# Performance work log

Hardware: AMD Instinct MI355X
Metric: run time of the kernel (lower is better)

The kernel has to match this reference:

```python
import jax, jax.numpy as jnp
import numpy as np

B, S, D, H, R, P = 4, 8192, 512, 8, 64, 4
HD = D // H  # 64
EPS = 1e-6


def _sketch_p4(z, G1, G2):
    # sketchwithnegativity(z, 2): M1 = M2 = z
    inv_sqrt_r = 1.0 / np.sqrt(R).astype(np.float32)
    half = inv_sqrt_r * ((z @ G1) * (z @ G2))  # [B,H,S,R]
    return half * half  # sketch(): half * half for p=4


def setup_inputs() -> dict:
    key = jax.random.key(0)
    ks = jax.random.split(key, 16)
    lin = lambda k: jax.random.normal(k, (D, D), jnp.float32) * (1.0 / np.sqrt(D))
    g = lambda k: jax.random.normal(k, (HD, R), jnp.float32) * (1.0 / np.sqrt(R))
    return {
        "x": jax.random.normal(ks[0], (B, S, D), jnp.float32),
        "Wq": lin(ks[1]), "bq": jnp.zeros((D,), jnp.float32),
        "Wk": lin(ks[2]), "bk": jnp.zeros((D,), jnp.float32),
        "Wv": lin(ks[3]), "bv": jnp.zeros((D,), jnp.float32),
        "Wp": lin(ks[4]), "bp": jnp.zeros((D,), jnp.float32),
        "gamma_q": jnp.ones((1,), jnp.float32), "beta_q": jnp.zeros((1,), jnp.float32),
        "gamma_k": jnp.ones((1,), jnp.float32), "beta_k": jnp.zeros((1,), jnp.float32),
        "qG1": g(ks[5]), "qG2": g(ks[6]),
        "kG1": g(ks[7]), "kG2": g(ks[8]),
    }


def reference(x, Wq, bq, Wk, bk, Wv, bv, Wp, bp,
              gamma_q, beta_q, gamma_k, beta_k, qG1, qG2, kG1, kG2):
    b, s, d = x.shape
    split = lambda t: t.reshape(b, s, H, HD).transpose(0, 2, 1, 3)  # [B,H,S,HD]
    q = split(x @ Wq + bq)
    k = split(x @ Wk + bk)
    v = split(x @ Wv + bv)
    q = gamma_q * q + beta_q
    k = gamma_k * k + beta_k
    phi_q = _sketch_p4(q, qG1, qG2)  # [B,H,S,R]
    phi_k = _sketch_p4(k, kG1, kG2)  # [B,H,S,R]
    # linear-attention form of attn = (phi_q phi_k^T) / rowsum; avoids [S,S]
    kv = jnp.einsum('bhsr,bhsd->bhrd', phi_k, v)          # [B,H,R,HD]
    ksum = phi_k.sum(axis=2)                              # [B,H,R]
    num = jnp.einsum('bhqr,bhrd->bhqd', phi_q, kv)        # [B,H,S,HD]
    den = jnp.einsum('bhqr,bhr->bhq', phi_q, ksum) + EPS  # [B,H,S]
    out = num / den[..., None]
    out = out.transpose(0, 2, 1, 3).reshape(b, s, d)
    return out @ Wp + bp
```

## Files before the change

kernel.cpp:

```cpp
#include <hip/hip_runtime.h>
#include <hip/hip_bf16.h>


#define SEQ 8192

typedef __attribute__((ext_vector_type(8))) short bf16x8;
typedef __attribute__((ext_vector_type(4))) float f32x4;

__device__ __forceinline__ unsigned short f2b(float f) {
    union { float f; unsigned int i; } v; v.f = f;
    unsigned int r = v.i + 0x7fffu + ((v.i >> 16) & 1u);
    return (unsigned short)(r >> 16);
}

#if __has_builtin(__builtin_amdgcn_global_load_lds)
#define ASYNC_CP 1
#endif

__device__ __forceinline__ void cp16(const unsigned short* g, unsigned short* l) {
#ifdef ASYNC_CP
    __builtin_amdgcn_global_load_lds(
        (const __attribute__((address_space(1))) unsigned int*)g,
        (__attribute__((address_space(3))) unsigned int*)l, 16, 0, 0);
#endif
}

__global__ __launch_bounds__(256) void convert_x(
    const float* __restrict__ x, unsigned short* __restrict__ xb)
{
    size_t i = ((size_t)blockIdx.x * 256 + threadIdx.x) * 8;
    float4 a = *(const float4*)&x[i];
    float4 b = *(const float4*)&x[i + 4];
    ushort4 o1 = { f2b(a.x), f2b(a.y), f2b(a.z), f2b(a.w) };
    ushort4 o2 = { f2b(b.x), f2b(b.y), f2b(b.z), f2b(b.w) };
    *(ushort4*)&xb[i]     = o1;
    *(ushort4*)&xb[i + 4] = o2;
}

__global__ __launch_bounds__(256) void convert_wT(
    const float* __restrict__ Wq, const float* __restrict__ Wk,
    const float* __restrict__ Wv, const float* __restrict__ Wp,
    unsigned short* __restrict__ WT)
{
    const int z = blockIdx.z;
    const float* W = (z == 0) ? Wq : (z == 1) ? Wk : (z == 2) ? Wv : Wp;
    unsigned short* O = WT + (size_t)z * 262144;
    __shared__ float t[32][33];
    const int tid = threadIdx.x;
    const int tx = tid & 31, ty = tid >> 5;
    const int k0 = blockIdx.x * 32, n0 = blockIdx.y * 32;
    #pragma unroll
    for (int i = 0; i < 4; ++i)
        t[ty + 8 * i][tx] = W[(size_t)(k0 + ty + 8 * i) * 512 + n0 + tx];
    __syncthreads();
    #pragma unroll
    for (int i = 0; i < 4; ++i)
        O[(size_t)(n0 + ty + 8 * i) * 512 + k0 + tx] = f2b(t[tx][ty + 8 * i]);
}

__global__ __launch_bounds__(256) void gemm_mfma_qkv(
    const unsigned short* __restrict__ xb,
    const unsigned short* __restrict__ WT,
    const float* __restrict__ bq, const float* __restrict__ bk,
    const float* __restrict__ bvp,
    const float* __restrict__ gq, const float* __restrict__ bbq,
    const float* __restrict__ gk, const float* __restrict__ bbk,
    float* __restrict__ Q, float* __restrict__ Ko, float* __restrict__ Vo)
{
    const int z = blockIdx.z;
    const unsigned short* Wt = WT + (size_t)z * 262144;
    const float* bias = (z == 0) ? bq : (z == 1) ? bk : bvp;
    float g = 1.0f, be = 0.0f;
    if (z == 0)      { g = gq[0]; be = bbq[0]; }
    else if (z == 1) { g = gk[0]; be = bbk[0]; }
    float* C = (z == 0) ? Q : (z == 1) ? Ko : Vo;

    __shared__ __align__(16) unsigned short As[128 * 32];
    __shared__ __align__(16) unsigned short Bs[128 * 32];

    const int tid = threadIdx.x;
    const int w = tid >> 6, lane = tid & 63;
    const int n0 = blockIdx.x * 128;
    const int j0 = blockIdx.y * 128;
    const int wr = w >> 1, wc = w & 1;

    const int r0 = w * 32 + (lane >> 2);
    const int kq = (lane & 3) * 8;
    const unsigned short* gA = &xb[(size_t)(n0 + r0) * 512 + kq];
    const unsigned short* gB = &Wt[(size_t)(j0 + r0) * 512 + kq];
    unsigned short* lA = &As[(w * 32) * 32];
    unsigned short* lB = &Bs[(w * 32) * 32];

    f32x4 acc[4][4];
    #pragma unroll
    for (int i = 0; i < 4; ++i)
        #pragma unroll
        for (int j = 0; j < 4; ++j) { acc[i][j] = (f32x4){0.f, 0.f, 0.f, 0.f}; }

    for (int k0 = 0; k0 < 512; k0 += 32) {
        __syncthreads();
#ifdef ASYNC_CP
        cp16(gA + k0, lA);
        cp16(gA + 16 * 512 + k0, lA + 16 * 32);
        cp16(gB + k0, lB);
        cp16(gB + 16 * 512 + k0, lB + 16 * 32);
#else
        { uint4 v = *(const uint4*)(gA + k0);            *(uint4*)(lA + (size_t)lane * 8) = v; }
        { uint4 v = *(const uint4*)(gA + 16 * 512 + k0); *(uint4*)(lA + 16 * 32 + (size_t)lane * 8) = v; }
        { uint4 v = *(const uint4*)(gB + k0);            *(uint4*)(lB + (size_t)lane * 8) = v; }
        { uint4 v = *(const uint4*)(gB + 16 * 512 + k0); *(uint4*)(lB + 16 * 32 + (size_t)lane * 8) = v; }
#endif
        __syncthreads();

        bf16x8 af[4], bfr[4];
        #pragma unroll
        for (int i = 0; i < 4; ++i) {
            af[i]  = *(const bf16x8*)&As[(wr * 64 + i * 16 + (lane & 15)) * 32 + (lane >> 4) * 8];
            bfr[i] = *(const bf16x8*)&Bs[(wc * 64 + i * 16 + (lane & 15)) * 32 + (lane >> 4) * 8];
        }
        #pragma unroll
        for (int mi = 0; mi < 4; ++mi)
            #pragma unroll
            for (int ni = 0; ni < 4; ++ni)
                acc[mi][ni] = __builtin_amdgcn_mfma_f32_16x16x32_bf16(
                    af[mi], bfr[ni], acc[mi][ni], 0, 0, 0);
    }

    #pragma unroll
    for (int ni = 0; ni < 4; ++ni) {
        const int jcol = j0 + wc * 64 + ni * 16 + (lane & 15);
        const float bv = bias[jcol];
        const int h = jcol >> 6, hd = jcol & 63;
        #pragma unroll
        for (int mi = 0; mi < 4; ++mi) {
            #pragma unroll
            for (int r = 0; r < 4; ++r) {
                const int t = n0 + wr * 64 + mi * 16 + (lane >> 4) * 4 + r;
                const int b = t >> 13, s = t & (SEQ - 1);
                C[(((size_t)(b * 8 + h)) * SEQ + s) * 64 + hd] =
                    fmaf(g, acc[mi][ni][r] + bv, be);
            }
        }
    }
}

__global__ __launch_bounds__(256) void gemm_mfma_final(
    const unsigned short* __restrict__ Ab,
    const unsigned short* __restrict__ WTp,
    const float* __restrict__ bias, float* __restrict__ out)
{
    __shared__ __align__(16) unsigned short As[128 * 32];
    __shared__ __align__(16) unsigned short Bs[128 * 32];

    const int tid = threadIdx.x;
    const int w = tid >> 6, lane = tid & 63;
    const int n0 = blockIdx.x * 128;
    const int j0 = blockIdx.y * 128;
    const int wr = w >> 1, wc = w & 1;

    const int r0 = w * 32 + (lane >> 2);
    const int kq = (lane & 3) * 8;
    const unsigned short* gA = &Ab[(size_t)(n0 + r0) * 512 + kq];
    const unsigned short* gB = &WTp[(size_t)(j0 + r0) * 512 + kq];
    unsigned short* lA = &As[(w * 32) * 32];
    unsigned short* lB = &Bs[(w * 32) * 32];

    f32x4 acc[4][4];
    #pragma unroll
    for (int i = 0; i < 4; ++i)
        #pragma unroll
        for (int j = 0; j < 4; ++j) { acc[i][j] = (f32x4){0.f, 0.f, 0.f, 0.f}; }

    for (int k0 = 0; k0 < 512; k0 += 32) {
        __syncthreads();
#ifdef ASYNC_CP
        cp16(gA + k0, lA);
        cp16(gA + 16 * 512 + k0, lA + 16 * 32);
        cp16(gB + k0, lB);
        cp16(gB + 16 * 512 + k0, lB + 16 * 32);
#else
        { uint4 v = *(const uint4*)(gA + k0);            *(uint4*)(lA + (size_t)lane * 8) = v; }
        { uint4 v = *(const uint4*)(gA + 16 * 512 + k0); *(uint4*)(lA + 16 * 32 + (size_t)lane * 8) = v; }
        { uint4 v = *(const uint4*)(gB + k0);            *(uint4*)(lB + (size_t)lane * 8) = v; }
        { uint4 v = *(const uint4*)(gB + 16 * 512 + k0); *(uint4*)(lB + 16 * 32 + (size_t)lane * 8) = v; }
#endif
        __syncthreads();

        bf16x8 af[4], bfr[4];
        #pragma unroll
        for (int i = 0; i < 4; ++i) {
            af[i]  = *(const bf16x8*)&As[(wr * 64 + i * 16 + (lane & 15)) * 32 + (lane >> 4) * 8];
            bfr[i] = *(const bf16x8*)&Bs[(wc * 64 + i * 16 + (lane & 15)) * 32 + (lane >> 4) * 8];
        }
        #pragma unroll
        for (int mi = 0; mi < 4; ++mi)
            #pragma unroll
            for (int ni = 0; ni < 4; ++ni)
                acc[mi][ni] = __builtin_amdgcn_mfma_f32_16x16x32_bf16(
                    af[mi], bfr[ni], acc[mi][ni], 0, 0, 0);
    }

    #pragma unroll
    for (int ni = 0; ni < 4; ++ni) {
        const int jcol = j0 + wc * 64 + ni * 16 + (lane & 15);
        const float bv = bias[jcol];
        #pragma unroll
        for (int mi = 0; mi < 4; ++mi) {
            #pragma unroll
            for (int r = 0; r < 4; ++r) {
                const int t = n0 + wr * 64 + mi * 16 + (lane >> 4) * 4 + r;
                out[(size_t)t * 512 + jcol] = acc[mi][ni][r] + bv;
            }
        }
    }
}

__global__ __launch_bounds__(256) void sketch_p4(
    float* __restrict__ Z,
    const float* __restrict__ G1, const float* __restrict__ G2)
{
    __shared__ float G1s[64][68];
    __shared__ float G2s[64][68];
    __shared__ float zs[64][65];
    const int tid = threadIdx.x;
    const int tx = tid & 15, ty = tid >> 4;
    const size_t base = (size_t)blockIdx.x * 4096;
    {
        const int r = tid >> 4, c4 = (tid & 15) * 4;
        #pragma unroll
        for (int it = 0; it < 4; ++it) {
            float4 g1 = *(const float4*)&G1[(r + 16 * it) * 64 + c4];
            float4 g2 = *(const float4*)&G2[(r + 16 * it) * 64 + c4];
            float4 zv = *(const float4*)&Z[base + (size_t)(r + 16 * it) * 64 + c4];
            *(float4*)&G1s[r + 16 * it][c4] = g1;
            *(float4*)&G2s[r + 16 * it][c4] = g2;
            zs[r + 16 * it][c4 + 0] = zv.x; zs[r + 16 * it][c4 + 1] = zv.y;
            zs[r + 16 * it][c4 + 2] = zv.z; zs[r + 16 * it][c4 + 3] = zv.w;
        }
    }
    __syncthreads();
    const int r0 = ty * 4, c0 = tx * 4;
    float u[4][4] = {}, w[4][4] = {};
    #pragma unroll 4
    for (int i = 0; i < 64; ++i) {
        float zr[4] = { zs[r0][i], zs[r0 + 1][i], zs[r0 + 2][i], zs[r0 + 3][i] };
        float4 g1 = *(const float4*)&G1s[i][c0];
        float4 g2 = *(const float4*)&G2s[i][c0];
        float g1a[4] = { g1.x, g1.y, g1.z, g1.w };
        float g2a[4] = { g2.x, g2.y, g2.z, g2.w };
        #pragma unroll
        for (int a = 0; a < 4; ++a)
            #pragma unroll
            for (int bb = 0; bb < 4; ++bb) {
                u[a][bb] = fmaf(zr[a], g1a[bb], u[a][bb]);
                w[a][bb] = fmaf(zr[a], g2a[bb], w[a][bb]);
            }
    }
    #pragma unroll
    for (int a = 0; a < 4; ++a) {
        float4 o;
        float h0 = 0.125f * u[a][0] * w[a][0]; o.x = h0 * h0;
        float h1 = 0.125f * u[a][1] * w[a][1]; o.y = h1 * h1;
        float h2 = 0.125f * u[a][2] * w[a][2]; o.z = h2 * h2;
        float h3 = 0.125f * u[a][3] * w[a][3]; o.w = h3 * h3;
        *(float4*)&Z[base + (size_t)(r0 + a) * 64 + c0] = o;
    }
}

__global__ __launch_bounds__(256) void kv_partial(
    const float* __restrict__ PHIK, const float* __restrict__ V,
    float* __restrict__ KVP, float* __restrict__ KSP)
{
    const int bh = blockIdx.x, ch = blockIdx.y;
    const float* phik = PHIK + ((size_t)bh * SEQ + ch * 256) * 64;
    const float* v    = V    + ((size_t)bh * SEQ + ch * 256) * 64;
    __shared__ float ps[64][68];
    __shared__ float vs[64][68];
    const int tid = threadIdx.x;
    const int tx = tid & 15, ty = tid >> 4;
    const int r0 = ty * 4, c0 = tx * 4;
    float acc[4][4] = {};
    float ks[4] = {};
    for (int sub = 0; sub < 4; ++sub) {
        __syncthreads();
        {
            const int r = tid >> 4, c4 = (tid & 15) * 4;
            #pragma unroll
            for (int it = 0; it < 4; ++it) {
                float4 p = *(const float4*)&phik[(size_t)(sub * 64 + r + 16 * it) * 64 + c4];
                float4 vv = *(const float4*)&v[(size_t)(sub * 64 + r + 16 * it) * 64 + c4];
                *(float4*)&ps[r + 16 * it][c4] = p;
                *(float4*)&vs[r + 16 * it][c4] = vv;
            }
        }
        __syncthreads();
        #pragma unroll 4
        for (int s = 0; s < 64; ++s) {
            float4 p4 = *(const float4*)&ps[s][r0];
            float4 v4 = *(const float4*)&vs[s][c0];
            float pa[4] = { p4.x, p4.y, p4.z, p4.w };
            float va[4] = { v4.x, v4.y, v4.z, v4.w };
            #pragma unroll
            for (int a = 0; a < 4; ++a) {
                ks[a] += pa[a];
                #pragma unroll
                for (int bb = 0; bb < 4; ++bb)
                    acc[a][bb] = fmaf(pa[a], va[bb], acc[a][bb]);
            }
        }
    }
    #pragma unroll
    for (int a = 0; a < 4; ++a) {
        float4 o = { acc[a][0], acc[a][1], acc[a][2], acc[a][3] };
        *(float4*)&KVP[((size_t)(bh * 32 + ch) * 64 + r0 + a) * 64 + c0] = o;
    }
    if (tx == 0) {
        #pragma unroll
        for (int a = 0; a < 4; ++a)
            KSP[(bh * 32 + ch) * 64 + r0 + a] = ks[a];
    }
}

__global__ __launch_bounds__(256) void kv_reduce(
    const float* __restrict__ KVP, const float* __restrict__ KSP,
    float* __restrict__ KV, float* __restrict__ KS)
{
    const int bh = blockIdx.x, tid = threadIdx.x;
    for (int e = tid; e < 4096; e += 256) {
        float s = 0.f;
        for (int c = 0; c < 32; ++c) s += KVP[(size_t)(bh * 32 + c) * 4096 + e];
        KV[(size_t)bh * 4096 + e] = s;
    }
    if (tid < 64) {
        float s = 0.f;
        for (int c = 0; c < 32; ++c) s += KSP[(bh * 32 + c) * 64 + tid];
        KS[bh * 64 + tid] = s;
    }
}

__global__ __launch_bounds__(256) void attn_out(
    const float* __restrict__ PHIQ, const float* __restrict__ KV,
    const float* __restrict__ KS, unsigned short* __restrict__ OAb)
{
    const int bh = blockIdx.x;
    const int b = bh >> 3, h = bh & 7;
    __shared__ float kvs[64][68];
    __shared__ float pqs[64][65];
    __shared__ float kss[64];
    const int tid = threadIdx.x;
    const int tx = tid & 15, ty = tid >> 4;
    const int s0 = blockIdx.y * 64;
    {
        const int r = tid >> 4, c4 = (tid & 15) * 4;
        #pragma unroll
        for (int it = 0; it < 4; ++it) {
            float4 kvv = *(const float4*)&KV[(size_t)bh * 4096 + (size_t)(r + 16 * it) * 64 + c4];
            float4 pq  = *(const float4*)&PHIQ[((size_t)bh * SEQ + s0 + r + 16 * it) * 64 + c4];
            *(float4*)&kvs[r + 16 * it][c4] = kvv;
            pqs[r + 16 * it][c4 + 0] = pq.x; pqs[r + 16 * it][c4 + 1] = pq.y;
            pqs[r + 16 * it][c4 + 2] = pq.z; pqs[r + 16 * it][c4 + 3] = pq.w;
        }
        if (tid < 64) kss[tid] = KS[bh * 64 + tid];
    }
    __syncthreads();
    const int r0 = ty * 4, c0 = tx * 4;
    float num[4][4] = {};
    float den[4] = { 1e-6f, 1e-6f, 1e-6f, 1e-6f };
    #pragma unroll 4
    for (int i = 0; i < 64; ++i) {
        float pr[4] = { pqs[r0][i], pqs[r0 + 1][i], pqs[r0 + 2][i], pqs[r0 + 3][i] };
        float4 kv4 = *(const float4*)&kvs[i][c0];
        float kva[4] = { kv4.x, kv4.y, kv4.z, kv4.w };
        float ksv = kss[i];
        #pragma unroll
        for (int a = 0; a < 4; ++a) {
            den[a] = fmaf(pr[a], ksv, den[a]);
            #pragma unroll
            for (int bb = 0; bb < 4; ++bb)
                num[a][bb] = fmaf(pr[a], kva[bb], num[a][bb]);
        }
    }
    #pragma unroll
    for (int a = 0; a < 4; ++a) {
        const float inv = 1.0f / den[a];
        ushort4 o = { f2b(num[a][0] * inv), f2b(num[a][1] * inv),
                      f2b(num[a][2] * inv), f2b(num[a][3] * inv) };
        const int s = s0 + r0 + a;
        *(ushort4*)&OAb[((size_t)(b * SEQ + s)) * 512 + h * 64 + c0] = o;
    }
}

extern "C" void kernel_launch(void* const* d_in, const int* in_sizes, int n_in,
                              void* d_out, int out_size, void* d_ws, size_t ws_size,
                              hipStream_t stream)
{
    (void)in_sizes; (void)n_in; (void)out_size; (void)ws_size;
    const float* x   = (const float*)d_in[0];
    const float* Wq  = (const float*)d_in[1];
    const float* bq  = (const float*)d_in[2];
    const float* Wk  = (const float*)d_in[3];
    const float* bk  = (const float*)d_in[4];
    const float* Wv  = (const float*)d_in[5];
    const float* bv  = (const float*)d_in[6];
    const float* Wp  = (const float*)d_in[7];
    const float* bp  = (const float*)d_in[8];
    const float* gq  = (const float*)d_in[9];
    const float* bbq = (const float*)d_in[10];
    const float* gk  = (const float*)d_in[11];
    const float* bbk = (const float*)d_in[12];
    const float* qG1 = (const float*)d_in[13];
    const float* qG2 = (const float*)d_in[14];
    const float* kG1 = (const float*)d_in[15];
    const float* kG2 = (const float*)d_in[16];

    float* ws  = (float*)d_ws;
    float* Q   = ws;
    float* Kb  = ws + 16777216;
    float* V   = ws + 2 * 16777216;
    float* R3  = ws + 3 * 16777216;
    unsigned short* xb  = (unsigned short*)R3;
    float* KVP = R3;
    float* KSP = R3 + 4194304;
    unsigned short* OAb = (unsigned short*)R3;
    float* KV  = ws + 3 * 16777216 + 8388608;
    float* KS  = KV + 131072;
    unsigned short* WT = (unsigned short*)(KS + 2048);
    float* out = (float*)d_out;

    hipLaunchKernelGGL(convert_x, dim3(8192), dim3(256), 0, stream, x, xb);
    hipLaunchKernelGGL(convert_wT, dim3(16, 16, 4), dim3(256), 0, stream,
                       Wq, Wk, Wv, Wp, WT);
    hipLaunchKernelGGL(gemm_mfma_qkv, dim3(256, 4, 3), dim3(256), 0, stream,
                       xb, WT, bq, bk, bv, gq, bbq, gk, bbk, Q, Kb, V);
    hipLaunchKernelGGL(sketch_p4, dim3(4096), dim3(256), 0, stream, Q, qG1, qG2);
    hipLaunchKernelGGL(sketch_p4, dim3(4096), dim3(256), 0, stream, Kb, kG1, kG2);
    hipLaunchKernelGGL(kv_partial, dim3(32, 32), dim3(256), 0, stream, Kb, V, KVP, KSP);
    hipLaunchKernelGGL(kv_reduce, dim3(32), dim3(256), 0, stream, KVP, KSP, KV, KS);
    hipLaunchKernelGGL(attn_out, dim3(32, 128), dim3(256), 0, stream, Q, KV, KS, OAb);
    hipLaunchKernelGGL(gemm_mfma_final, dim3(256, 4), dim3(256), 0, stream,
                       OAb, WT + 3 * 262144, bp, out);
}
```

Measured before the change: 477.5 us.

## Fold sketch projections into QKV weights and fuse sketch into GEMM epilogue

Precomputes combined weights W·G (with gamma/beta/bias folded into a column bias) so one GEMM directly produces both sketch projections per head. The epilogue pairs adjacent columns via lane shuffle to form phi = (u·w/8)^2 and writes it in bf16, removing the separate sketch kernels and the fp32 Q/K intermediates. V and phi are stored as bf16, halving intermediate traffic for kv_partial and attn_out. The GEMM N width grows from 1536 to 2560, and bf16 storage of phi (a fourth power) adds precision risk.

```diff
diff --git a/kernel.cpp b/kernel.cpp
--- a/kernel.cpp
+++ b/kernel.cpp
@@ -11,6 +11,9 @@
     union { float f; unsigned int i; } v; v.f = f;
     unsigned int r = v.i + 0x7fffu + ((v.i >> 16) & 1u);
     return (unsigned short)(r >> 16);
+}
+__device__ __forceinline__ float b2f(unsigned short u) {
+    union { unsigned int i; float f; } v; v.i = ((unsigned int)u) << 16; return v.f;
 }
 
 #if __has_builtin(__builtin_amdgcn_global_load_lds)
@@ -38,13 +41,12 @@
 }
 
 __global__ __launch_bounds__(256) void convert_wT(
-    const float* __restrict__ Wq, const float* __restrict__ Wk,
     const float* __restrict__ Wv, const float* __restrict__ Wp,
-    unsigned short* __restrict__ WT)
+    unsigned short* __restrict__ WTf, unsigned short* __restrict__ WTp)
 {
     const int z = blockIdx.z;
-    const float* W = (z == 0) ? Wq : (z == 1) ? Wk : (z == 2) ? Wv : Wp;
-    unsigned short* O = WT + (size_t)z * 262144;
+    const float* W = (z == 0) ? Wv : Wp;
+    unsigned short* O = (z == 0) ? (WTf + (size_t)2048 * 512) : WTp;
     __shared__ float t[32][33];
     const int tid = threadIdx.x;
     const int tx = tid & 31, ty = tid >> 5;
@@ -58,23 +60,60 @@
         O[(size_t)(n0 + ty + 8 * i) * 512 + k0 + tx] = f2b(t[tx][ty + 8 * i]);
 }
 
-__global__ __launch_bounds__(256) void gemm_mfma_qkv(
-    const unsigned short* __restrict__ xb,
-    const unsigned short* __restrict__ WT,
-    const float* __restrict__ bq, const float* __restrict__ bk,
-    const float* __restrict__ bvp,
+__global__ __launch_bounds__(256) void precompute_wc(
+    const float* __restrict__ Wq, const float* __restrict__ bq,
+    const float* __restrict__ Wk, const float* __restrict__ bk,
+    const float* __restrict__ bv,
     const float* __restrict__ gq, const float* __restrict__ bbq,
     const float* __restrict__ gk, const float* __restrict__ bbk,
-    float* __restrict__ Q, float* __restrict__ Ko, float* __restrict__ Vo)
-{
-    const int z = blockIdx.z;
-    const unsigned short* Wt = WT + (size_t)z * 262144;
-    const float* bias = (z == 0) ? bq : (z == 1) ? bk : bvp;
-    float g = 1.0f, be = 0.0f;
-    if (z == 0)      { g = gq[0]; be = bbq[0]; }
-    else if (z == 1) { g = gk[0]; be = bbk[0]; }
-    float* C = (z == 0) ? Q : (z == 1) ? Ko : Vo;
-
+    const float* __restrict__ qG1, const float* __restrict__ qG2,
+    const float* __restrict__ kG1, const float* __restrict__ kG2,
+    unsigned short* __restrict__ WTf, float* __restrict__ cvec)
+{
+    const int bi = blockIdx.x;
+    const int tid = threadIdx.x;
+    if (bi == 32) {
+        for (int i = tid; i < 512; i += 256) cvec[2048 + i] = bv[i];
+        return;
+    }
+    const int zz = bi >> 4, h = (bi >> 1) & 7, p = bi & 1;
+    const float* W    = zz ? Wk : Wq;
+    const float* bias = zz ? bk : bq;
+    const float* G    = zz ? (p ? kG2 : kG1) : (p ? qG2 : qG1);
+    const float  gamma = zz ? gk[0] : gq[0];
+    const float  beta  = zz ? bbk[0] : bbq[0];
+
+    __shared__ float Gs[64][65];
+    for (int i = tid; i < 4096; i += 256) Gs[i >> 6][i & 63] = G[i];
+    __syncthreads();
+
+    const int rr = tid & 63, kg = tid >> 6;
+    const int jc = zz * 1024 + h * 128 + rr * 2 + p;
+    for (int k = kg; k < 512; k += 4) {
+        float s = 0.f;
+        const float* wrow = &W[(size_t)k * 512 + h * 64];
+        #pragma unroll 8
+        for (int j = 0; j < 64; ++j) s = fmaf(wrow[j], Gs[j][rr], s);
+        WTf[(size_t)jc * 512 + k] = f2b(gamma * s);
+    }
+    if (kg == 0) {
+        float cb = 0.f, cg = 0.f;
+        #pragma unroll 8
+        for (int j = 0; j < 64; ++j) {
+            cb = fmaf(bias[h * 64 + j], Gs[j][rr], cb);
+            cg += Gs[j][rr];
+        }
+        cvec[jc] = gamma * cb + beta * cg;
+    }
+}
+
+__global__ __launch_bounds__(256) void gemm_mfma_fused(
+    const unsigned short* __restrict__ xb,
+    const unsigned short* __restrict__ WTf,
+    const float* __restrict__ cvec,
+    unsigned short* __restrict__ PHIQ, unsigned short* __restrict__ PHIK,
+    unsigned short* __restrict__ Vb)
+{
     __shared__ __align__(16) unsigned short As[128 * 32];
     __shared__ __align__(16) unsigned short Bs[128 * 32];
 
@@ -87,7 +126,7 @@
     const int r0 = w * 32 + (lane >> 2);
     const int kq = (lane & 3) * 8;
     const unsigned short* gA = &xb[(size_t)(n0 + r0) * 512 + kq];
-    const unsigned short* gB = &Wt[(size_t)(j0 + r0) * 512 + kq];
+    const unsigned short* gB = &WTf[(size_t)(j0 + r0) * 512 + kq];
     unsigned short* lA = &As[(w * 32) * 32];
     unsigned short* lB = &Bs[(w * 32) * 32];
 
@@ -129,16 +168,39 @@
     #pragma unroll
     for (int ni = 0; ni < 4; ++ni) {
         const int jcol = j0 + wc * 64 + ni * 16 + (lane & 15);
-        const float bv = bias[jcol];
-        const int h = jcol >> 6, hd = jcol & 63;
-        #pragma unroll
-        for (int mi = 0; mi < 4; ++mi) {
-            #pragma unroll
-            for (int r = 0; r < 4; ++r) {
-                const int t = n0 + wr * 64 + mi * 16 + (lane >> 4) * 4 + r;
-                const int b = t >> 13, s = t & (SEQ - 1);
-                C[(((size_t)(b * 8 + h)) * SEQ + s) * 64 + hd] =
-                    fmaf(g, acc[mi][ni][r] + bv, be);
+        const float cv = cvec[jcol];
+        if (jcol < 2048) {
+            const int zq = jcol >> 10;
+            const int lc = jcol & 1023;
+            const int h = lc >> 7, rr = (lc >> 1) & 63;
+            unsigned short* dst = zq ? PHIK : PHIQ;
+            #pragma unroll
+            for (int mi = 0; mi < 4; ++mi) {
+                #pragma unroll
+                for (int r = 0; r < 4; ++r) {
+                    float u = acc[mi][ni][r] + cv;
+                    float up = __shfl_xor(u, 1);
+                    float hh = 0.125f * u * up;
+                    float phi = hh * hh;
+                    if ((lane & 1) == 0) {
+                        const int t = n0 + wr * 64 + mi * 16 + (lane >> 4) * 4 + r;
+                        const int b = t >> 13, s = t & (SEQ - 1);
+                        dst[((size_t)(b * 8 + h) * SEQ + s) * 64 + rr] = f2b(phi);
+                    }
+                }
+            }
+        } else {
+            const int n = jcol - 2048;
+            const int h = n >> 6, hd = n & 63;
+            #pragma unroll
+            for (int mi = 0; mi < 4; ++mi) {
+                #pragma unroll
+                for (int r = 0; r < 4; ++r) {
+                    const int t = n0 + wr * 64 + mi * 16 + (lane >> 4) * 4 + r;
+                    const int b = t >> 13, s = t & (SEQ - 1);
+                    Vb[((size_t)(b * 8 + h) * SEQ + s) * 64 + hd] =
+                        f2b(acc[mi][ni][r] + cv);
+                }
             }
         }
     }
@@ -203,77 +265,25 @@
     #pragma unroll
     for (int ni = 0; ni < 4; ++ni) {
         const int jcol = j0 + wc * 64 + ni * 16 + (lane & 15);
-        const float bv = bias[jcol];
+        const float bvv = bias[jcol];
         #pragma unroll
         for (int mi = 0; mi < 4; ++mi) {
             #pragma unroll
             for (int r = 0; r < 4; ++r) {
                 const int t = n0 + wr * 64 + mi * 16 + (lane >> 4) * 4 + r;
-                out[(size_t)t * 512 + jcol] = acc[mi][ni][r] + bv;
+                out[(size_t)t * 512 + jcol] = acc[mi][ni][r] + bvv;
             }
         }
     }
 }
 
-__global__ __launch_bounds__(256) void sketch_p4(
-    float* __restrict__ Z,
-    const float* __restrict__ G1, const float* __restrict__ G2)
-{
-    __shared__ float G1s[64][68];
-    __shared__ float G2s[64][68];
-    __shared__ float zs[64][65];
-    const int tid = threadIdx.x;
-    const int tx = tid & 15, ty = tid >> 4;
-    const size_t base = (size_t)blockIdx.x * 4096;
-    {
-        const int r = tid >> 4, c4 = (tid & 15) * 4;
-        #pragma unroll
-        for (int it = 0; it < 4; ++it) {
-            float4 g1 = *(const float4*)&G1[(r + 16 * it) * 64 + c4];
-            float4 g2 = *(const float4*)&G2[(r + 16 * it) * 64 + c4];
-            float4 zv = *(const float4*)&Z[base + (size_t)(r + 16 * it) * 64 + c4];
-            *(float4*)&G1s[r + 16 * it][c4] = g1;
-            *(float4*)&G2s[r + 16 * it][c4] = g2;
-            zs[r + 16 * it][c4 + 0] = zv.x; zs[r + 16 * it][c4 + 1] = zv.y;
-            zs[r + 16 * it][c4 + 2] = zv.z; zs[r + 16 * it][c4 + 3] = zv.w;
-        }
-    }
-    __syncthreads();
-    const int r0 = ty * 4, c0 = tx * 4;
-    float u[4][4] = {}, w[4][4] = {};
-    #pragma unroll 4
-    for (int i = 0; i < 64; ++i) {
-        float zr[4] = { zs[r0][i], zs[r0 + 1][i], zs[r0 + 2][i], zs[r0 + 3][i] };
-        float4 g1 = *(const float4*)&G1s[i][c0];
-        float4 g2 = *(const float4*)&G2s[i][c0];
-        float g1a[4] = { g1.x, g1.y, g1.z, g1.w };
-        float g2a[4] = { g2.x, g2.y, g2.z, g2.w };
-        #pragma unroll
-        for (int a = 0; a < 4; ++a)
-            #pragma unroll
-            for (int bb = 0; bb < 4; ++bb) {
-                u[a][bb] = fmaf(zr[a], g1a[bb], u[a][bb]);
-                w[a][bb] = fmaf(zr[a], g2a[bb], w[a][bb]);
-            }
-    }
-    #pragma unroll
-    for (int a = 0; a < 4; ++a) {
-        float4 o;
-        float h0 = 0.125f * u[a][0] * w[a][0]; o.x = h0 * h0;
-        float h1 = 0.125f * u[a][1] * w[a][1]; o.y = h1 * h1;
-        float h2 = 0.125f * u[a][2] * w[a][2]; o.z = h2 * h2;
-        float h3 = 0.125f * u[a][3] * w[a][3]; o.w = h3 * h3;
-        *(float4*)&Z[base + (size_t)(r0 + a) * 64 + c0] = o;
-    }
-}
-
 __global__ __launch_bounds__(256) void kv_partial(
-    const float* __restrict__ PHIK, const float* __restrict__ V,
+    const unsigned short* __restrict__ PHIK, const unsigned short* __restrict__ Vb,
     float* __restrict__ KVP, float* __restrict__ KSP)
 {
     const int bh = blockIdx.x, ch = blockIdx.y;
-    const float* phik = PHIK + ((size_t)bh * SEQ + ch * 256) * 64;
-    const float* v    = V    + ((size_t)bh * SEQ + ch * 256) * 64;
+    const unsigned short* phik = PHIK + ((size_t)bh * SEQ + ch * 256) * 64;
+    const unsigned short* v    = Vb   + ((size_t)bh * SEQ + ch * 256) * 64;
     __shared__ float ps[64][68];
     __shared__ float vs[64][68];
     const int tid = threadIdx.x;
@@ -287,10 +297,12 @@
             const int r = tid >> 4, c4 = (tid & 15) * 4;
             #pragma unroll
             for (int it = 0; it < 4; ++it) {
-                float4 p = *(const float4*)&phik[(size_t)(sub * 64 + r + 16 * it) * 64 + c4];
-                float4 vv = *(const float4*)&v[(size_t)(sub * 64 + r + 16 * it) * 64 + c4];
-                *(float4*)&ps[r + 16 * it][c4] = p;
-                *(float4*)&vs[r + 16 * it][c4] = vv;
+                ushort4 p = *(const ushort4*)&phik[(size_t)(sub * 64 + r + 16 * it) * 64 + c4];
+                ushort4 vv = *(const ushort4*)&v[(size_t)(sub * 64 + r + 16 * it) * 64 + c4];
+                ps[r + 16 * it][c4 + 0] = b2f(p.x);  ps[r + 16 * it][c4 + 1] = b2f(p.y);
+                ps[r + 16 * it][c4 + 2] = b2f(p.z);  ps[r + 16 * it][c4 + 3] = b2f(p.w);
+                vs[r + 16 * it][c4 + 0] = b2f(vv.x); vs[r + 16 * it][c4 + 1] = b2f(vv.y);
+                vs[r + 16 * it][c4 + 2] = b2f(vv.z); vs[r + 16 * it][c4 + 3] = b2f(vv.w);
             }
         }
         __syncthreads();
@@ -339,7 +351,7 @@
 }
 
 __global__ __launch_bounds__(256) void attn_out(
-    const float* __restrict__ PHIQ, const float* __restrict__ KV,
+    const unsigned short* __restrict__ PHIQ, const float* __restrict__ KV,
     const float* __restrict__ KS, unsigned short* __restrict__ OAb)
 {
     const int bh = blockIdx.x;
@@ -355,10 +367,10 @@
         #pragma unroll
         for (int it = 0; it < 4; ++it) {
             float4 kvv = *(const float4*)&KV[(size_t)bh * 4096 + (size_t)(r + 16 * it) * 64 + c4];
-            float4 pq  = *(const float4*)&PHIQ[((size_t)bh * SEQ + s0 + r + 16 * it) * 64 + c4];
+            ushort4 pq = *(const ushort4*)&PHIQ[((size_t)bh * SEQ + s0 + r + 16 * it) * 64 + c4];
             *(float4*)&kvs[r + 16 * it][c4] = kvv;
-            pqs[r + 16 * it][c4 + 0] = pq.x; pqs[r + 16 * it][c4 + 1] = pq.y;
-            pqs[r + 16 * it][c4 + 2] = pq.z; pqs[r + 16 * it][c4 + 3] = pq.w;
+            pqs[r + 16 * it][c4 + 0] = b2f(pq.x); pqs[r + 16 * it][c4 + 1] = b2f(pq.y);
+            pqs[r + 16 * it][c4 + 2] = b2f(pq.z); pqs[r + 16 * it][c4 + 3] = b2f(pq.w);
         }
         if (tid < 64) kss[tid] = KS[bh * 64 + tid];
     }
@@ -413,30 +425,33 @@
     const float* kG1 = (const float*)d_in[15];
     const float* kG2 = (const float*)d_in[16];
 
-    float* ws  = (float*)d_ws;
-    float* Q   = ws;
-    float* Kb  = ws + 16777216;
-    float* V   = ws + 2 * 16777216;
-    float* R3  = ws + 3 * 16777216;
-    unsigned short* xb  = (unsigned short*)R3;
-    float* KVP = R3;
-    float* KSP = R3 + 4194304;
-    unsigned short* OAb = (unsigned short*)R3;
-    float* KV  = ws + 3 * 16777216 + 8388608;
-    float* KS  = KV + 131072;
-    unsigned short* WT = (unsigned short*)(KS + 2048);
-    float* out = (float*)d_out;
+    unsigned short* PHIQ = (unsigned short*)d_ws;
+    unsigned short* PHIK = PHIQ + 16777216;
+    unsigned short* Vb   = PHIK + 16777216;
+    unsigned short* xb   = Vb   + 16777216;
+    unsigned short* OAb  = xb   + 16777216;
+    unsigned short* WTf  = OAb  + 16777216;
+    unsigned short* WTp  = WTf  + 2560 * 512;
+    float* cvec = (float*)(WTp + 262144);
+    float* KVP  = cvec + 2560;
+    float* KSP  = KVP + 4194304;
+    float* KV   = KSP + 65536;
+    float* KS   = KV + 131072;
+    float* out  = (float*)d_out;
 
     hipLaunchKernelGGL(convert_x, dim3(8192), dim3(256), 0, stream, x, xb);
-    hipLaunchKernelGGL(convert_wT, dim3(16, 16, 4), dim3(256), 0, stream,
-                       Wq, Wk, Wv, Wp, WT);
-    hipLaunchKernelGGL(gemm_mfma_qkv, dim3(256, 4, 3), dim3(256), 0, stream,
-                       xb, WT, bq, bk, bv, gq, bbq, gk, bbk, Q, Kb, V);
-    hipLaunchKernelGGL(sketch_p4, dim3(4096), dim3(256), 0, stream, Q, qG1, qG2);
-    hipLaunchKernelGGL(sketch_p4, dim3(4096), dim3(256), 0, stream, Kb, kG1, kG2);
-    hipLaunchKernelGGL(kv_partial, dim3(32, 32), dim3(256), 0, stream, Kb, V, KVP, KSP);
+    hipLaunchKernelGGL(convert_wT, dim3(16, 16, 2), dim3(256), 0, stream,
+                       Wv, Wp, WTf, WTp);
+    hipLaunchKernelGGL(precompute_wc, dim3(33), dim3(256), 0, stream,
+                       Wq, bq, Wk, bk, bv, gq, bbq, gk, bbk,
+                       qG1, qG2, kG1, kG2, WTf, cvec);
+    hipLaunchKernelGGL(gemm_mfma_fused, dim3(256, 20), dim3(256), 0, stream,
+                       xb, WTf, cvec, PHIQ, PHIK, Vb);
+    hipLaunchKernelGGL(kv_partial, dim3(32, 32), dim3(256), 0, stream,
+                       PHIK, Vb, KVP, KSP);
     hipLaunchKernelGGL(kv_reduce, dim3(32), dim3(256), 0, stream, KVP, KSP, KV, KS);
-    hipLaunchKernelGGL(attn_out, dim3(32, 128), dim3(256), 0, stream, Q, KV, KS, OAb);
+    hipLaunchKernelGGL(attn_out, dim3(32, 128), dim3(256), 0, stream,
+                       PHIQ, KV, KS, OAb);
     hipLaunchKernelGGL(gemm_mfma_final, dim3(256, 4), dim3(256), 0, stream,
-                       OAb, WT + 3 * 262144, bp, out);
-}
+                       OAb, WTp, bp, out);
+}
```

Result: slower. 576.5 us (+20.7%).
